# Performance work log

Measured on AMD Instinct MI355X. Metric: run time of the kernel, lower is better.

The kernel has to match this reference:

```python
import jax, jax.numpy as jnp
import numpy as np

B, C, H, W = 4, 256, 128, 128
D = 256            # attention hidden_dim (== C, so no output_proj)
HID = 1024         # mlp hidden = int(C * 4.0)
EPS = 1e-5


def setup_inputs() -> dict:
    key = jax.random.key(0)
    ks = jax.random.split(key, 16)
    s = 0.02
    return {
        "x": jax.random.normal(ks[0], (B, C, H, W), jnp.float32),
        "wq": jax.random.normal(ks[1], (C, D), jnp.float32) * s,
        "bq": jnp.zeros((D,), jnp.float32),
        "wk": jax.random.normal(ks[2], (C, D), jnp.float32) * s,
        "bk": jnp.zeros((D,), jnp.float32),
        "wv": jax.random.normal(ks[3], (C, D), jnp.float32) * s,
        "bv": jnp.zeros((D,), jnp.float32),
        "ln1_g": jnp.ones((C,), jnp.float32),
        "ln1_b": jnp.zeros((C,), jnp.float32),
        "ln2_g": jnp.ones((C,), jnp.float32),
        "ln2_b": jnp.zeros((C,), jnp.float32),
        "fc1_w": jax.random.normal(ks[4], (C, HID), jnp.float32) * s,
        "fc1_b": jnp.zeros((HID,), jnp.float32),
        "fc2_w": jax.random.normal(ks[5], (HID, C), jnp.float32) * s,
        "fc2_b": jnp.zeros((C,), jnp.float32),
    }


def _layernorm(x, g, b):
    m = jnp.mean(x, axis=-1, keepdims=True)
    v = jnp.mean(jnp.square(x - m), axis=-1, keepdims=True)
    return (x - m) * jax.lax.rsqrt(v + EPS) * g + b


def _neighborhoods(t):
    # t: [B,H,W,D] -> [B,H,W,9,D] 3x3 neighborhoods, zero-padded at borders
    tp = jnp.pad(t, ((0, 0), (1, 1), (1, 1), (0, 0)))
    h, w = t.shape[1], t.shape[2]
    return jnp.stack(
        [tp[:, dy:dy + h, dx:dx + w, :] for dy in range(3) for dx in range(3)],
        axis=3,
    )


def _valid_mask(h, w):
    # [H,W,9] bool: which of the 9 neighbors are inside the grid
    ys = jnp.arange(h)[:, None] * jnp.ones((1, w), jnp.int32)
    xs = jnp.arange(w)[None, :] * jnp.ones((h, 1), jnp.int32)
    top, bot = ys > 0, ys < h - 1
    lef, rig = xs > 0, xs < w - 1
    ones = jnp.ones((h, w), bool)
    return jnp.stack(
        [top & lef, top, top & rig, lef, ones, rig, bot & lef, bot, bot & rig],
        axis=-1,
    )


def reference(x, wq, bq, wk, bk, wv, bv, ln1_g, ln1_b, ln2_g, ln2_b,
              fc1_w, fc1_b, fc2_w, fc2_b):
    b_, c_, h_, w_ = x.shape
    xc = jnp.transpose(x, (0, 2, 3, 1))                    # [B,H,W,C]
    n1 = _layernorm(xc, ln1_g, ln1_b)
    q = n1 @ wq + bq                                       # [B,H,W,D]
    k = n1 @ wk + bk
    v = n1 @ wv + bv
    kn = _neighborhoods(k)                                  # [B,H,W,9,D]
    vn = _neighborhoods(v)
    scores = jnp.einsum('bhwd,bhwnd->bhwn', q, kn) / jnp.sqrt(jnp.float32(q.shape[-1]))
    mask = _valid_mask(h_, w_)                               # [H,W,9]
    scores = jnp.where(mask, scores, jnp.float32(-1e9))
    weights = jax.nn.softmax(scores, axis=-1)
    attn = jnp.einsum('bhwn,bhwnd->bhwd', weights, vn)       # [B,H,W,D]
    x1 = xc + attn                                           # residual 1
    n2 = _layernorm(x1, ln2_g, ln2_b)
    mlp = jax.nn.gelu(n2 @ fc1_w + fc1_b, approximate=False) @ fc2_w + fc2_b
    out = x1 + mlp
    return jnp.transpose(out, (0, 3, 1, 2))                  # [B,C,H,W]
```

## Files before the change

kernel.cpp:

```cpp
#include <hip/hip_runtime.h>
#include <hip/hip_bf16.h>
#include <math.h>

#define NPIX  65536
#define CCH   256
#define HWSZ  16384
#define WIDTH 128
#define HID   1024

typedef unsigned short u16;
typedef __bf16 bf16x8 __attribute__((ext_vector_type(8)));
typedef float  floatx4 __attribute__((ext_vector_type(4)));

__device__ __forceinline__ float bf2f(u16 u) {
  union { unsigned int i; float f; } c; c.i = ((unsigned int)u) << 16; return c.f;
}
__device__ __forceinline__ float bflo(unsigned int u) {
  union { unsigned int i; float f; } c; c.i = u << 16; return c.f;
}
__device__ __forceinline__ float bfhi(unsigned int u) {
  union { unsigned int i; float f; } c; c.i = u & 0xffff0000u; return c.f;
}
__device__ __forceinline__ u16 f2bf(float f) {
  union { float f; unsigned int i; } c; c.f = f;
  unsigned int x = c.i;
  x += 0x7fffu + ((x >> 16) & 1u);
  return (u16)(x >> 16);
}
__device__ __forceinline__ float gelu_tanh(float val) {
  const float t = 0.7978845608028654f * (val + 0.044715f * val * val * val);
  const float e = __expf(2.0f * t);
  const float th = 1.0f - 2.0f / (e + 1.0f);
  return 0.5f * val * (1.0f + th);
}

__device__ __forceinline__ void async16(const void* g, void* l) {
  __builtin_amdgcn_global_load_lds(
      (const __attribute__((address_space(1))) void*)g,
      (__attribute__((address_space(3))) void*)l, 16, 0, 0);
}

__global__ __launch_bounds__(256) void wfrag_kernel(
    const float* __restrict__ src, u16* __restrict__ dst, int N, int K) {
  const int tid = threadIdx.x;
  const int u = blockIdx.x * 4 + (tid >> 6);
  const int lane = tid & 63, quad = lane >> 4, l16 = lane & 15;
  const int K32 = K >> 5;
  const int g = u / K32, kb = u - g * K32;
  const int n = g * 16 + l16;
  const int k0 = kb * 32 + quad * 8;
  u16 tmp[8];
#pragma unroll
  for (int e = 0; e < 8; e++) tmp[e] = f2bf(src[(size_t)(k0 + e) * N + n]);
  *(bf16x8*)(dst + ((size_t)u * 64 + lane) * 8) = *(bf16x8*)tmp;
}

__global__ __launch_bounds__(256) void concat_bias_kernel(
    const float* __restrict__ bq, const float* __restrict__ bk,
    const float* __restrict__ bv, float* __restrict__ dst) {
  const int i = blockIdx.x * 256 + threadIdx.x;
  if (i < 256) dst[i] = bq[i];
  else if (i < 512) dst[i] = bk[i - 256];
  else if (i < 768) dst[i] = bv[i - 512];
}

__global__ __launch_bounds__(256) void ln1_kernel(
    const float* __restrict__ x, const float* __restrict__ g,
    const float* __restrict__ bb, u16* __restrict__ n1) {
  __shared__ float sx[32][257];
  __shared__ float sred[16][32];
  __shared__ float sm[32], sr[32];
  const int tx = threadIdx.x;
  const int p0 = blockIdx.x * 32;
  {
    const int pix = tx & 31, cpart = tx >> 5;
    const int p = p0 + pix;
    const int b = p >> 14, hw = p & (HWSZ - 1);
    const float* xb = x + ((size_t)b * CCH) * HWSZ + hw;
    float s = 0.f, s2 = 0.f;
#pragma unroll 4
    for (int i = 0; i < 32; i++) {
      const int c = cpart * 32 + i;
      const float v = xb[(size_t)c * HWSZ];
      sx[pix][c] = v;
      s += v; s2 += v * v;
    }
    sred[cpart][pix] = s; sred[8 + cpart][pix] = s2;
  }
  __syncthreads();
  if (tx < 32) {
    float s = 0.f, s2 = 0.f;
#pragma unroll
    for (int j = 0; j < 8; j++) { s += sred[j][tx]; s2 += sred[8 + j][tx]; }
    const float m = s * (1.0f / 256.0f);
    const float var = s2 * (1.0f / 256.0f) - m * m;
    sm[tx] = m; sr[tx] = rsqrtf(var + 1e-5f);
  }
  __syncthreads();
  const float gc = g[tx], bc = bb[tx];
#pragma unroll 4
  for (int i = 0; i < 32; i++) {
    const float v = (sx[i][tx] - sm[i]) * sr[i] * gc + bc;
    n1[(size_t)(p0 + i) * CCH + tx] = f2bf(v);
  }
}

__global__ __launch_bounds__(256) void res_ln2_kernel(
    const float* __restrict__ x, const u16* __restrict__ attn,
    const float* __restrict__ g, const float* __restrict__ bb,
    float* __restrict__ x1, u16* __restrict__ n2) {
  __shared__ float sx[32][257];
  __shared__ float sred[16][32];
  __shared__ float sm[32], sr[32];
  const int tx = threadIdx.x;
  const int p0 = blockIdx.x * 32;
  {
    const int pix = tx & 31, cpart = tx >> 5;
    const int p = p0 + pix;
    const int b = p >> 14, hw = p & (HWSZ - 1);
    const float* xb = x + ((size_t)b * CCH) * HWSZ + hw;
#pragma unroll 4
    for (int i = 0; i < 32; i++) {
      const int c = cpart * 32 + i;
      sx[pix][c] = xb[(size_t)c * HWSZ];
    }
  }
  __syncthreads();
#pragma unroll 4
  for (int i = 0; i < 32; i++) {
    const float v = sx[i][tx] + bf2f(attn[(size_t)(p0 + i) * CCH + tx]);
    sx[i][tx] = v;
    x1[(size_t)(p0 + i) * CCH + tx] = v;
  }
  __syncthreads();
  {
    const int pix = tx & 31, cpart = tx >> 5;
    float s = 0.f, s2 = 0.f;
#pragma unroll 4
    for (int i = 0; i < 32; i++) {
      const float v = sx[pix][cpart * 32 + i];
      s += v; s2 += v * v;
    }
    sred[cpart][pix] = s; sred[8 + cpart][pix] = s2;
  }
  __syncthreads();
  if (tx < 32) {
    float s = 0.f, s2 = 0.f;
#pragma unroll
    for (int j = 0; j < 8; j++) { s += sred[j][tx]; s2 += sred[8 + j][tx]; }
    const float m = s * (1.0f / 256.0f);
    const float var = s2 * (1.0f / 256.0f) - m * m;
    sm[tx] = m; sr[tx] = rsqrtf(var + 1e-5f);
  }
  __syncthreads();
  const float gc = g[tx], bc = bb[tx];
#pragma unroll 4
  for (int i = 0; i < 32; i++) {
    const float v = (sx[i][tx] - sm[i]) * sr[i] * gc + bc;
    n2[(size_t)(p0 + i) * CCH + tx] = f2bf(v);
  }
}

__global__ __launch_bounds__(256) void attn_kernel(
    const u16* __restrict__ qkv, u16* __restrict__ attn) {
  const int tid = threadIdx.x;
  const int wave = tid >> 6, lane = tid & 63;
  const int p = blockIdx.x * 4 + wave;
  const int hw = p & (HWSZ - 1);
  const int hh = hw >> 7, ww = hw & (WIDTH - 1);
  const u16* rowp = qkv + (size_t)p * 768 + lane * 4;
  const uint2 qr = *(const uint2*)rowp;
  const float qf0 = bflo(qr.x), qf1 = bfhi(qr.x);
  const float qf2 = bflo(qr.y), qf3 = bfhi(qr.y);
  float sc[9];
#pragma unroll
  for (int n = 0; n < 9; n++) {
    const int dy = n / 3 - 1, dx = n % 3 - 1;
    const int y = hh + dy, x2 = ww + dx;
    float s = -1e30f;
    if (y >= 0 && y < 128 && x2 >= 0 && x2 < 128) {
      const uint2 kr = *(const uint2*)(rowp + 256 + (dy * WIDTH + dx) * 768);
      float d = qf0 * bflo(kr.x) + qf1 * bfhi(kr.x)
              + qf2 * bflo(kr.y) + qf3 * bfhi(kr.y);
#pragma unroll
      for (int o = 32; o >= 1; o >>= 1) d += __shfl_xor(d, o, 64);
      s = d * 0.0625f;
    }
    sc[n] = s;
  }
  float mx = sc[0];
#pragma unroll
  for (int n = 1; n < 9; n++) mx = fmaxf(mx, sc[n]);
  float wgt[9], wsum = 0.f;
#pragma unroll
  for (int n = 0; n < 9; n++) { wgt[n] = __expf(sc[n] - mx); wsum += wgt[n]; }
  const float inv = 1.0f / wsum;
  float a0 = 0.f, a1 = 0.f, a2 = 0.f, a3 = 0.f;
#pragma unroll
  for (int n = 0; n < 9; n++) {
    const int dy = n / 3 - 1, dx = n % 3 - 1;
    const int y = hh + dy, x2 = ww + dx;
    if (y >= 0 && y < 128 && x2 >= 0 && x2 < 128) {
      const uint2 vr = *(const uint2*)(rowp + 512 + (dy * WIDTH + dx) * 768);
      const float wn = wgt[n] * inv;
      a0 += wn * bflo(vr.x); a1 += wn * bfhi(vr.x);
      a2 += wn * bflo(vr.y); a3 += wn * bfhi(vr.y);
    }
  }
  uint2 o;
  o.x = ((unsigned int)f2bf(a1) << 16) | (unsigned int)f2bf(a0);
  o.y = ((unsigned int)f2bf(a3) << 16) | (unsigned int)f2bf(a2);
  *(uint2*)(attn + (size_t)p * CCH + lane * 4) = o;
}

template <int NCH, int NST, int EPI>
__global__ __launch_bounds__(256, 3) void gemm_blds(
    const u16* __restrict__ A, const u16* __restrict__ wf,
    const float* __restrict__ bias, u16* __restrict__ outb) {
  __shared__ u16 sB[2][16384];
  const int tid  = threadIdx.x;
  const int wave = tid >> 6, lane = tid & 63;
  const int quad = lane >> 4, l16 = lane & 15;
  const int m0 = blockIdx.x * 128 + wave * 32;

  const u16* aRow = A + (size_t)(m0 + l16) * CCH + quad * 8;
  bf16x8 afr[2][8];
#pragma unroll
  for (int mi = 0; mi < 2; mi++)
#pragma unroll
    for (int ks = 0; ks < 8; ks++)
      afr[mi][ks] = *(const bf16x8*)(aRow + (size_t)mi * 16 * CCH + ks * 32);

  auto stage = [&](int ch, int buf) {
    const u16* g = wf + (size_t)ch * 16384;
#pragma unroll
    for (int i = 0; i < 8; i++)
      async16(g + i * 2048 + tid * 8, &sB[buf][i * 2048 + tid * 8]);
  };

  stage(0, 0);
#pragma unroll 1
  for (int ch = 0; ch < NCH; ++ch) {
    __syncthreads();
    if (ch + 1 < NCH) stage(ch + 1, (ch + 1) & 1);
    const u16* sb = sB[ch & 1];
    floatx4 acc[2][4];
#pragma unroll
    for (int mi = 0; mi < 2; mi++)
#pragma unroll
      for (int gi = 0; gi < 4; gi++) acc[mi][gi] = (floatx4){0.f, 0.f, 0.f, 0.f};
#pragma unroll
    for (int ks = 0; ks < 8; ks++) {
      bf16x8 bfr[4];
#pragma unroll
      for (int gi = 0; gi < 4; gi++)
        bfr[gi] = *(const bf16x8*)&sb[(gi * 8 + ks) * 512 + lane * 8];
#pragma unroll
      for (int mi = 0; mi < 2; mi++)
#pragma unroll
        for (int gi = 0; gi < 4; gi++)
          acc[mi][gi] = __builtin_amdgcn_mfma_f32_16x16x32_bf16(
              afr[mi][ks], bfr[gi], acc[mi][gi], 0, 0, 0);
    }
#pragma unroll
    for (int mi = 0; mi < 2; mi++)
#pragma unroll
      for (int gi = 0; gi < 4; gi++) {
        const int col = ch * 64 + gi * 16 + l16;
        const float bs = bias[col];
        const int row0 = m0 + mi * 16 + quad * 4;
#pragma unroll
        for (int r = 0; r < 4; r++) {
          float val = acc[mi][gi][r] + bs;
          if constexpr (EPI == 1) val = gelu_tanh(val);
          outb[(size_t)(row0 + r) * NST + col] = f2bf(val);
        }
      }
  }
}

__global__ __launch_bounds__(256, 3) void fc2_kernel(
    const u16* __restrict__ h, const u16* __restrict__ f2F,
    const float* __restrict__ bias, const float* __restrict__ x1,
    float* __restrict__ out) {
  __shared__ u16 sB[2][8192];
  const int tid  = threadIdx.x;
  const int wave = tid >> 6, lane = tid & 63;
  const int quad = lane >> 4, l16 = lane & 15;
  const int bx = blockIdx.x;
  const int m0 = (bx >> 1) * 128 + (wave & 1) * 64;
  const int nb = bx & 1;
  const int wgi = (wave >> 1) * 4;

  const u16* aRow = h + (size_t)(m0 + l16) * HID + quad * 8;

  auto stage = [&](int kc, int buf) {
#pragma unroll
    for (int i = 0; i < 4; i++) {
      const int s = i * 256 + tid;
      const int gl = s >> 7;
      const int rem = s & 127;
      async16(f2F + (((size_t)(nb * 8 + gl) * 32 + kc * 2) << 9) + rem * 8,
              &sB[buf][s * 8]);
    }
  };

  floatx4 acc[4][4];
#pragma unroll
  for (int mi = 0; mi < 4; mi++)
#pragma unroll
    for (int gi = 0; gi < 4; gi++) acc[mi][gi] = (floatx4){0.f, 0.f, 0.f, 0.f};

  stage(0, 0);
#pragma unroll 1
  for (int kc = 0; kc < 16; ++kc) {
    bf16x8 afr[4][2];
#pragma unroll
    for (int mi = 0; mi < 4; mi++)
#pragma unroll
      for (int ks = 0; ks < 2; ks++)
        afr[mi][ks] = *(const bf16x8*)(aRow + (size_t)mi * 16 * HID + kc * 64 + ks * 32);
    __syncthreads();
    if (kc + 1 < 16) stage(kc + 1, (kc + 1) & 1);
    const u16* sb = sB[kc & 1];
#pragma unroll
    for (int ks = 0; ks < 2; ks++) {
      bf16x8 bfr[4];
#pragma unroll
      for (int gi = 0; gi < 4; gi++)
        bfr[gi] = *(const bf16x8*)&sb[((wgi + gi) * 2 + ks) * 512 + lane * 8];
#pragma unroll
      for (int mi = 0; mi < 4; mi++)
#pragma unroll
        for (int gi = 0; gi < 4; gi++)
          acc[mi][gi] = __builtin_amdgcn_mfma_f32_16x16x32_bf16(
              afr[mi][ks], bfr[gi], acc[mi][gi], 0, 0, 0);
    }
  }

#pragma unroll
  for (int mi = 0; mi < 4; mi++)
#pragma unroll
    for (int gi = 0; gi < 4; gi++) {
      const int col = nb * 128 + (wgi + gi) * 16 + l16;
      const float bs = bias[col];
      const int row0 = m0 + mi * 16 + quad * 4;
      floatx4 vv;
#pragma unroll
      for (int r = 0; r < 4; r++)
        vv[r] = acc[mi][gi][r] + bs + x1[(size_t)(row0 + r) * CCH + col];
      *(floatx4*)&out[((size_t)((row0 >> 14) * CCH + col)) * HWSZ + (row0 & (HWSZ - 1))] = vv;
    }
}

extern "C" void kernel_launch(void* const* d_in, const int* in_sizes, int n_in,
                              void* d_out, int out_size, void* d_ws, size_t ws_size,
                              hipStream_t stream) {
  const float* x    = (const float*)d_in[0];
  const float* wq   = (const float*)d_in[1];
  const float* bq   = (const float*)d_in[2];
  const float* wk   = (const float*)d_in[3];
  const float* bk   = (const float*)d_in[4];
  const float* wv   = (const float*)d_in[5];
  const float* bv   = (const float*)d_in[6];
  const float* ln1g = (const float*)d_in[7];
  const float* ln1b = (const float*)d_in[8];
  const float* ln2g = (const float*)d_in[9];
  const float* ln2b = (const float*)d_in[10];
  const float* fc1w = (const float*)d_in[11];
  const float* fc1b = (const float*)d_in[12];
  const float* fc2w = (const float*)d_in[13];
  const float* fc2b = (const float*)d_in[14];
  float* out = (float*)d_out;

  char* ws = (char*)d_ws;
  const size_t MB = (size_t)1 << 20;
  float* x1   = (float*)(ws);
  u16* qkv    = (u16*)(ws + 64 * MB);
  u16* hbuf   = (u16*)(ws + 64 * MB);
  u16* n1     = (u16*)(ws + 160 * MB);
  u16* attnb  = n1;
  u16* n2     = (u16*)(ws + 192 * MB);
  u16* wqkvF  = (u16*)(ws + 224 * MB);
  u16* f1F    = wqkvF + 768 * 256;
  u16* f2F    = f1F + 1024 * 256;
  float* bqkv = (float*)(f2F + 256 * 1024);

  dim3 blk(256);
  wfrag_kernel<<<dim3(32),  blk, 0, stream>>>(wq,   wqkvF,          256, 256);
  wfrag_kernel<<<dim3(32),  blk, 0, stream>>>(wk,   wqkvF + 65536,  256, 256);
  wfrag_kernel<<<dim3(32),  blk, 0, stream>>>(wv,   wqkvF + 131072, 256, 256);
  wfrag_kernel<<<dim3(128), blk, 0, stream>>>(fc1w, f1F, 1024, 256);
  wfrag_kernel<<<dim3(128), blk, 0, stream>>>(fc2w, f2F, 256, 1024);
  concat_bias_kernel<<<dim3(3), blk, 0, stream>>>(bq, bk, bv, bqkv);

  ln1_kernel<<<NPIX / 32, blk, 0, stream>>>(x, ln1g, ln1b, n1);

  gemm_blds<12, 768, 0><<<dim3(NPIX / 128), blk, 0, stream>>>(n1, wqkvF, bqkv, qkv);

  attn_kernel<<<NPIX / 4, blk, 0, stream>>>(qkv, attnb);

  res_ln2_kernel<<<NPIX / 32, blk, 0, stream>>>(x, attnb, ln2g, ln2b, x1, n2);

  gemm_blds<16, 1024, 1><<<dim3(NPIX / 128), blk, 0, stream>>>(n2, f1F, fc1b, hbuf);

  fc2_kernel<<<dim3((NPIX / 128) * 2), blk, 0, stream>>>(hbuf, f2F, fc2b, x1, out);
}
```

Baseline: 482.4 us.

## Enlarge GEMM warp tiles to 64x64 and make fc2 blocks cover full N

The QKV and FC1 GEMMs now keep a 64-row A slice per wave in registers and compute 64x64 output per wave over 128-column N tiles, with the B tiles staged in K-chunks. The old scheme had 32-row waves over 64-column chunks. FC2 now has each block compute all 256 output columns, so the A (hidden activations) reads are no longer duplicated across two blocks, and A fragments are double-buffered in registers to overlap loads with MFMA. This raises MFMA work per LDS read and cuts redundant global reads. In exchange it uses more registers, lowers the occupancy target to 2, and adds more barriers per tile.

```diff
diff --git a/kernel.cpp b/kernel.cpp
--- a/kernel.cpp
+++ b/kernel.cpp
@@ -213,73 +213,84 @@
   *(uint2*)(attn + (size_t)p * CCH + lane * 4) = o;
 }
 
-template <int NCH, int NST, int EPI>
-__global__ __launch_bounds__(256, 3) void gemm_blds(
+template <int NT, int NST, int GELU>
+__global__ __launch_bounds__(256, 2) void gemm_areg(
     const u16* __restrict__ A, const u16* __restrict__ wf,
     const float* __restrict__ bias, u16* __restrict__ outb) {
-  __shared__ u16 sB[2][16384];
+  __shared__ u16 sB[2][8192];
   const int tid  = threadIdx.x;
   const int wave = tid >> 6, lane = tid & 63;
   const int quad = lane >> 4, l16 = lane & 15;
-  const int m0 = blockIdx.x * 128 + wave * 32;
-
-  const u16* aRow = A + (size_t)(m0 + l16) * CCH + quad * 8;
-  bf16x8 afr[2][8];
-#pragma unroll
-  for (int mi = 0; mi < 2; mi++)
-#pragma unroll
-    for (int ks = 0; ks < 8; ks++)
-      afr[mi][ks] = *(const bf16x8*)(aRow + (size_t)mi * 16 * CCH + ks * 32);
-
-  auto stage = [&](int ch, int buf) {
-    const u16* g = wf + (size_t)ch * 16384;
-#pragma unroll
-    for (int i = 0; i < 8; i++)
-      async16(g + i * 2048 + tid * 8, &sB[buf][i * 2048 + tid * 8]);
+  const int m0  = blockIdx.x * 128;
+  const int wr  = (wave & 1) * 64;
+  const int wgl = (wave >> 1) * 4;
+
+  const u16* aRow = A + (size_t)(m0 + wr + l16) * CCH + quad * 8;
+  bf16x8 afr[4][8];
+#pragma unroll
+  for (int mi = 0; mi < 4; mi++)
+#pragma unroll
+    for (int k8 = 0; k8 < 8; k8++)
+      afr[mi][k8] = *(const bf16x8*)(aRow + (size_t)mi * 16 * CCH + k8 * 32);
+
+  auto stage = [&](int t, int buf) {
+    const int nt = t >> 2, kc = t & 3;
+#pragma unroll
+    for (int i = 0; i < 4; i++) {
+      const int s = i * 256 + tid;
+      const int u = s >> 6;
+      const int g = nt * 8 + (u >> 1);
+      const int kb = kc * 2 + (u & 1);
+      async16(wf + (((size_t)g * 8 + kb) << 9) + (s & 63) * 8, &sB[buf][s * 8]);
+    }
   };
 
   stage(0, 0);
 #pragma unroll 1
-  for (int ch = 0; ch < NCH; ++ch) {
-    __syncthreads();
-    if (ch + 1 < NCH) stage(ch + 1, (ch + 1) & 1);
-    const u16* sb = sB[ch & 1];
-    floatx4 acc[2][4];
-#pragma unroll
-    for (int mi = 0; mi < 2; mi++)
+  for (int nt = 0; nt < NT; ++nt) {
+    floatx4 acc[4][4];
+#pragma unroll
+    for (int mi = 0; mi < 4; mi++)
 #pragma unroll
       for (int gi = 0; gi < 4; gi++) acc[mi][gi] = (floatx4){0.f, 0.f, 0.f, 0.f};
 #pragma unroll
-    for (int ks = 0; ks < 8; ks++) {
-      bf16x8 bfr[4];
-#pragma unroll
-      for (int gi = 0; gi < 4; gi++)
-        bfr[gi] = *(const bf16x8*)&sb[(gi * 8 + ks) * 512 + lane * 8];
-#pragma unroll
-      for (int mi = 0; mi < 2; mi++)
+    for (int kc = 0; kc < 4; ++kc) {
+      const int t = nt * 4 + kc;
+      __syncthreads();
+      if (t + 1 < NT * 4) stage(t + 1, (kc + 1) & 1);
+      const u16* sb = sB[kc & 1];
+#pragma unroll
+      for (int ks = 0; ks < 2; ++ks) {
+        bf16x8 bfr[4];
 #pragma unroll
         for (int gi = 0; gi < 4; gi++)
-          acc[mi][gi] = __builtin_amdgcn_mfma_f32_16x16x32_bf16(
-              afr[mi][ks], bfr[gi], acc[mi][gi], 0, 0, 0);
-    }
-#pragma unroll
-    for (int mi = 0; mi < 2; mi++)
+          bfr[gi] = *(const bf16x8*)&sb[((wgl + gi) * 2 + ks) * 512 + lane * 8];
+#pragma unroll
+        for (int mi = 0; mi < 4; mi++)
+#pragma unroll
+          for (int gi = 0; gi < 4; gi++)
+            acc[mi][gi] = __builtin_amdgcn_mfma_f32_16x16x32_bf16(
+                afr[mi][kc * 2 + ks], bfr[gi], acc[mi][gi], 0, 0, 0);
+      }
+    }
+#pragma unroll
+    for (int mi = 0; mi < 4; mi++)
 #pragma unroll
       for (int gi = 0; gi < 4; gi++) {
-        const int col = ch * 64 + gi * 16 + l16;
+        const int col = nt * 128 + (wave >> 1) * 64 + gi * 16 + l16;
         const float bs = bias[col];
-        const int row0 = m0 + mi * 16 + quad * 4;
+        const int row0 = m0 + wr + mi * 16 + quad * 4;
 #pragma unroll
         for (int r = 0; r < 4; r++) {
           float val = acc[mi][gi][r] + bs;
-          if constexpr (EPI == 1) val = gelu_tanh(val);
+          if constexpr (GELU) val = gelu_tanh(val);
           outb[(size_t)(row0 + r) * NST + col] = f2bf(val);
         }
       }
   }
 }
 
-__global__ __launch_bounds__(256, 3) void fc2_kernel(
+__global__ __launch_bounds__(256, 2) void fc2_kernel(
     const u16* __restrict__ h, const u16* __restrict__ f2F,
     const float* __restrict__ bias, const float* __restrict__ x1,
     float* __restrict__ out) {
@@ -287,70 +298,93 @@
   const int tid  = threadIdx.x;
   const int wave = tid >> 6, lane = tid & 63;
   const int quad = lane >> 4, l16 = lane & 15;
-  const int bx = blockIdx.x;
-  const int m0 = (bx >> 1) * 128 + (wave & 1) * 64;
-  const int nb = bx & 1;
-  const int wgi = (wave >> 1) * 4;
-
-  const u16* aRow = h + (size_t)(m0 + l16) * HID + quad * 8;
-
-  auto stage = [&](int kc, int buf) {
+  const int m0  = blockIdx.x * 128;
+  const int wr  = (wave & 1) * 64;
+  const int wgl = (wave >> 1) * 4;
+
+  const u16* aRow = h + (size_t)(m0 + wr + l16) * HID + quad * 8;
+
+  bf16x8 afrA[4][2], afrB[4][2];
+  auto loadA = [&](int kc, bf16x8 (&af)[4][2]) {
+#pragma unroll
+    for (int mi = 0; mi < 4; mi++)
+#pragma unroll
+      for (int ks = 0; ks < 2; ks++)
+        af[mi][ks] = *(const bf16x8*)(aRow + (size_t)mi * 16 * HID + kc * 64 + ks * 32);
+  };
+  auto stage = [&](int t, int buf) {
+    const int kc = t >> 1, nt = t & 1;
 #pragma unroll
     for (int i = 0; i < 4; i++) {
       const int s = i * 256 + tid;
-      const int gl = s >> 7;
-      const int rem = s & 127;
-      async16(f2F + (((size_t)(nb * 8 + gl) * 32 + kc * 2) << 9) + rem * 8,
-              &sB[buf][s * 8]);
+      const int u = s >> 6;
+      const int g = nt * 8 + (u >> 1);
+      const int kb = kc * 2 + (u & 1);
+      async16(f2F + (((size_t)g * 32 + kb) << 9) + (s & 63) * 8, &sB[buf][s * 8]);
     }
   };
 
-  floatx4 acc[4][4];
-#pragma unroll
-  for (int mi = 0; mi < 4; mi++)
-#pragma unroll
-    for (int gi = 0; gi < 4; gi++) acc[mi][gi] = (floatx4){0.f, 0.f, 0.f, 0.f};
-
+  floatx4 acc[2][4][4];
+#pragma unroll
+  for (int nt = 0; nt < 2; nt++)
+#pragma unroll
+    for (int mi = 0; mi < 4; mi++)
+#pragma unroll
+      for (int gi = 0; gi < 4; gi++) acc[nt][mi][gi] = (floatx4){0.f, 0.f, 0.f, 0.f};
+
+  auto compute = [&](bf16x8 (&af)[4][2], int buf, int nt) {
+    const u16* sb = sB[buf];
+#pragma unroll
+    for (int ks = 0; ks < 2; ++ks) {
+      bf16x8 bfr[4];
+#pragma unroll
+      for (int gi = 0; gi < 4; gi++)
+        bfr[gi] = *(const bf16x8*)&sb[((wgl + gi) * 2 + ks) * 512 + lane * 8];
+#pragma unroll
+      for (int mi = 0; mi < 4; mi++)
+#pragma unroll
+        for (int gi = 0; gi < 4; gi++)
+          acc[nt][mi][gi] = __builtin_amdgcn_mfma_f32_16x16x32_bf16(
+              af[mi][ks], bfr[gi], acc[nt][mi][gi], 0, 0, 0);
+    }
+  };
+
+  loadA(0, afrA);
   stage(0, 0);
 #pragma unroll 1
-  for (int kc = 0; kc < 16; ++kc) {
-    bf16x8 afr[4][2];
+  for (int kc2 = 0; kc2 < 8; ++kc2) {
+    const int t0 = kc2 * 4;
+    __syncthreads();
+    stage(t0 + 1, 1);
+    loadA(2 * kc2 + 1, afrB);
+    compute(afrA, 0, 0);
+    __syncthreads();
+    stage(t0 + 2, 0);
+    compute(afrA, 1, 1);
+    __syncthreads();
+    stage(t0 + 3, 1);
+    if (kc2 + 1 < 8) loadA(2 * kc2 + 2, afrA);
+    compute(afrB, 0, 0);
+    __syncthreads();
+    if (t0 + 4 < 32) stage(t0 + 4, 0);
+    compute(afrB, 1, 1);
+  }
+
+#pragma unroll
+  for (int nt = 0; nt < 2; nt++)
 #pragma unroll
     for (int mi = 0; mi < 4; mi++)
 #pragma unroll
-      for (int ks = 0; ks < 2; ks++)
-        afr[mi][ks] = *(const bf16x8*)(aRow + (size_t)mi * 16 * HID + kc * 64 + ks * 32);
-    __syncthreads();
-    if (kc + 1 < 16) stage(kc + 1, (kc + 1) & 1);
-    const u16* sb = sB[kc & 1];
-#pragma unroll
-    for (int ks = 0; ks < 2; ks++) {
-      bf16x8 bfr[4];
-#pragma unroll
-      for (int gi = 0; gi < 4; gi++)
-        bfr[gi] = *(const bf16x8*)&sb[((wgi + gi) * 2 + ks) * 512 + lane * 8];
-#pragma unroll
-      for (int mi = 0; mi < 4; mi++)
-#pragma unroll
-        for (int gi = 0; gi < 4; gi++)
-          acc[mi][gi] = __builtin_amdgcn_mfma_f32_16x16x32_bf16(
-              afr[mi][ks], bfr[gi], acc[mi][gi], 0, 0, 0);
-    }
-  }
-
-#pragma unroll
-  for (int mi = 0; mi < 4; mi++)
-#pragma unroll
-    for (int gi = 0; gi < 4; gi++) {
-      const int col = nb * 128 + (wgi + gi) * 16 + l16;
-      const float bs = bias[col];
-      const int row0 = m0 + mi * 16 + quad * 4;
-      floatx4 vv;
-#pragma unroll
-      for (int r = 0; r < 4; r++)
-        vv[r] = acc[mi][gi][r] + bs + x1[(size_t)(row0 + r) * CCH + col];
-      *(floatx4*)&out[((size_t)((row0 >> 14) * CCH + col)) * HWSZ + (row0 & (HWSZ - 1))] = vv;
-    }
+      for (int gi = 0; gi < 4; gi++) {
+        const int col = nt * 128 + (wave >> 1) * 64 + gi * 16 + l16;
+        const float bs = bias[col];
+        const int row0 = m0 + wr + mi * 16 + quad * 4;
+        floatx4 vv;
+#pragma unroll
+        for (int r = 0; r < 4; r++)
+          vv[r] = acc[nt][mi][gi][r] + bs + x1[(size_t)(row0 + r) * CCH + col];
+        *(floatx4*)&out[((size_t)((row0 >> 14) * CCH + col)) * HWSZ + (row0 & (HWSZ - 1))] = vv;
+      }
 }
 
 extern "C" void kernel_launch(void* const* d_in, const int* in_sizes, int n_in,
@@ -396,13 +430,13 @@
 
   ln1_kernel<<<NPIX / 32, blk, 0, stream>>>(x, ln1g, ln1b, n1);
 
-  gemm_blds<12, 768, 0><<<dim3(NPIX / 128), blk, 0, stream>>>(n1, wqkvF, bqkv, qkv);
+  gemm_areg<6, 768, 0><<<dim3(NPIX / 128), blk, 0, stream>>>(n1, wqkvF, bqkv, qkv);
 
   attn_kernel<<<NPIX / 4, blk, 0, stream>>>(qkv, attnb);
 
   res_ln2_kernel<<<NPIX / 32, blk, 0, stream>>>(x, attnb, ln2g, ln2b, x1, n2);
 
-  gemm_blds<16, 1024, 1><<<dim3(NPIX / 128), blk, 0, stream>>>(n2, f1F, fc1b, hbuf);
-
-  fc2_kernel<<<dim3((NPIX / 128) * 2), blk, 0, stream>>>(hbuf, f2F, fc2b, x1, out);
-}
+  gemm_areg<8, 1024, 1><<<dim3(NPIX / 128), blk, 0, stream>>>(n2, f1F, fc1b, hbuf);
+
+  fc2_kernel<<<dim3(NPIX / 128), blk, 0, stream>>>(hbuf, f2F, fc2b, x1, out);
+}
```

Result: slower. 493.0 us (+2.2%).
